# Performance work log

Measured on AMD Instinct MI355X. Metric: run time of the kernel, lower is better.

The kernel has to match this reference:

```python
import jax, jax.numpy as jnp
import numpy as np

A, E, O = 8, 4096, 256          # agents, envs-per-agent, obs dim
H1, H2, H3 = 1024, 1024, 512     # idims
S = 4                            # number of shared (SEPS) networks


def setup_inputs() -> dict:
    key = jax.random.key(0)
    ks = jax.random.split(key, 8)
    f32 = jnp.float32
    return {
        "x": jax.random.normal(ks[0], (A, E, O), f32),
        "W1": jax.random.normal(ks[1], (S, O, H1), f32) * (1.0 / np.sqrt(O)),
        "b1": jnp.zeros((S, H1), f32),
        "W2": jax.random.normal(ks[2], (S, H1, H2), f32) * (np.sqrt(2.0) / np.sqrt(H1)),
        "b2": jnp.zeros((S, H2), f32),
        "W3": jax.random.normal(ks[3], (S, H2, H3), f32) * (np.sqrt(2.0) / np.sqrt(H2)),
        "b3": jnp.zeros((S, H3), f32),
        "seps_idx": jax.random.randint(ks[4], (A,), 0, S, dtype=jnp.int64),
    }


def reference(x, W1, b1, W2, b2, W3, b3, seps_idx):
    # x: [A, E, O]. Each of the S nets is applied (as in the original Python
    # loop) to the full stacked input, then the per-agent output is gathered
    # by seps_idx. MLP: Linear -> ReLU -> Linear -> ReLU -> Linear.
    def mlp(w1, bb1, w2, bb2, w3, bb3):
        h = jax.nn.relu(jnp.einsum('aeo,oh->aeh', x, w1) + bb1)
        h = jax.nn.relu(jnp.einsum('aeh,hg->aeg', h, w2) + bb2)
        return jnp.einsum('aeg,gk->aek', h, w3) + bb3

    out = jax.vmap(mlp)(W1, b1, W2, b2, W3, b3)           # [S, A, E, H3]
    sel = out[seps_idx, jnp.arange(A)]                    # [A, E, H3]
    return sel
```

## Files before the change

kernel.cpp:

```cpp
#include <hip/hip_runtime.h>
#include <hip/hip_bf16.h>


typedef unsigned short u16;
typedef __bf16 bf16x8 __attribute__((ext_vector_type(8)));
typedef float floatx4 __attribute__((ext_vector_type(4)));
typedef unsigned short ushort8 __attribute__((ext_vector_type(8)));

__device__ __forceinline__ u16 f2bf(float f) {
    union { float f; unsigned int u; } v; v.f = f;
    unsigned int u = v.u;
    return (u16)((u + 0x7FFFu + ((u >> 16) & 1u)) >> 16);
}

__device__ __forceinline__ void load16(const void* g, void* l) {
    __builtin_amdgcn_global_load_lds(
        (const __attribute__((address_space(1))) void*)(unsigned long long)g,
        (__attribute__((address_space(3))) void*)(unsigned int)(unsigned long long)l,
        16, 0, 0);
}

__global__ __launch_bounds__(256) void prep(
    const float* __restrict__ x, u16* __restrict__ xb,
    const float* __restrict__ W1, u16* __restrict__ w1t,
    const float* __restrict__ W2, u16* __restrict__ w2t,
    const float* __restrict__ W3, u16* __restrict__ w3t) {
    __shared__ float tile[32][33];
    int b = blockIdx.x;
    const int tid = threadIdx.x;
    if (b < 8192) {
        int i = (b * 256 + tid) * 4;
        float4 v = *(const float4*)(x + i);
        ushort4 o;
        o.x = f2bf(v.x); o.y = f2bf(v.y); o.z = f2bf(v.z); o.w = f2bf(v.w);
        *(ushort4*)(xb + i) = o;
        return;
    }
    b -= 8192;
    const float* src; u16* dst; int K, N, n0, k0, s;
    if (b < 1024) {
        s = b >> 8; int r = b & 255;
        K = 256; N = 1024; n0 = (r & 31) * 32; k0 = (r >> 5) * 32;
        src = W1; dst = w1t;
    } else if (b < 5120) {
        b -= 1024; s = b >> 10; int r = b & 1023;
        K = 1024; N = 1024; n0 = (r & 31) * 32; k0 = (r >> 5) * 32;
        src = W2; dst = w2t;
    } else {
        b -= 5120; s = b >> 9; int r = b & 511;
        K = 1024; N = 512; n0 = (r & 15) * 32; k0 = (r >> 4) * 32;
        src = W3; dst = w3t;
    }
    src += (size_t)s * K * N;
    dst += (size_t)s * N * K;
    const int tx = tid & 31, ty = tid >> 5;
#pragma unroll
    for (int j = 0; j < 32; j += 8)
        tile[ty + j][tx] = src[(size_t)(k0 + ty + j) * N + (n0 + tx)];
    __syncthreads();
#pragma unroll
    for (int j = 0; j < 32; j += 8)
        dst[(size_t)(n0 + ty + j) * K + (k0 + tx)] = f2bf(tile[tx][ty + j]);
}

template <int K, int N, bool RELU, bool OUT_BF16>
__global__ __launch_bounds__(512, 2) void gemm_mlp(
    const u16* __restrict__ Amat, const u16* __restrict__ Wt,
    const float* __restrict__ bias, const int* __restrict__ seps,
    void* __restrict__ outp) {
    constexpr int BM = 256, BK = 32;
    constexpr int NT = K / BK;
    constexpr int NHT = 4 * NT;
    constexpr int NNB = N / 256;
    constexpr int LNB = (NNB == 4) ? 2 : 1;
    extern __shared__ u16 lds[];

    const int tid = threadIdx.x;
    const int wave = tid >> 6, lane = tid & 63;
    const int wm = wave >> 2, wn = wave & 3;
    const int quad = lane >> 4, l16 = lane & 15;

    const int bidx = blockIdx.x;
    const int t = bidx >> 3;
    const int mb = (t >> LNB) * 8 + (bidx & 7);
    const int nb = t & (NNB - 1);
    const int m0 = mb * BM, n0 = nb * 256;

    const int s = seps[m0 >> 12];
    const u16* Ab = Amat + (size_t)m0 * K;
    const u16* Bb = Wt + ((size_t)s * N + n0) * K;

    const int soff = ((wave << 4) + (lane >> 2)) * K
                   + (((lane & 3) ^ ((lane >> 2) & 3)) << 3);
    u16* const ldsw = &lds[wave << 9];

    auto STAGE = [&](int sh) {
        if (sh < NHT) {
            const int tl = sh >> 2, ht = sh & 3;
            const u16* g = (ht & 2) ? Bb : Ab;
            if (ht & 1) g += 128 * K;
            load16(g + tl * BK + soff, ldsw + ((tl & 3) << 14) + (ht << 12));
        }
    };

    floatx4 acc[8][4];
#pragma unroll
    for (int i = 0; i < 8; ++i)
#pragma unroll
        for (int j = 0; j < 4; ++j) acc[i][j] = (floatx4){0.f, 0.f, 0.f, 0.f};

#pragma unroll
    for (int sh = 0; sh < 8; ++sh) STAGE(sh);
    asm volatile("s_waitcnt vmcnt(4)" ::: "memory");
    __builtin_amdgcn_s_barrier();

    const int aslot = (quad ^ (l16 & 3)) << 3;
    const int arow = (wm << 7) + l16;
    const int brow = (wn << 6) + l16;

#pragma unroll 1
    for (int T = 0; T < NT; ++T) {
        const u16* buf = &lds[(T & 3) << 14];
        const int sb = (T + 2) << 2;
        bf16x8 bfr[4];
#pragma unroll
        for (int q = 0; q < 2; ++q) {
            bf16x8 af[4];
#pragma unroll
            for (int i = 0; i < 4; ++i)
                af[i] = *(const bf16x8*)&buf[((arow + (q << 6) + (i << 4)) << 5) + aslot];
            if (q == 0) {
#pragma unroll
                for (int nf = 0; nf < 4; ++nf)
                    bfr[nf] = *(const bf16x8*)&buf[8192 + ((brow + (nf << 4)) << 5) + aslot];
            }
            STAGE(sb + (q << 1));
            STAGE(sb + (q << 1) + 1);
            if (q == 1) {
                if (T < NT - 2) asm volatile("s_waitcnt vmcnt(4)" ::: "memory");
                else            asm volatile("s_waitcnt vmcnt(0)" ::: "memory");
            }
            __builtin_amdgcn_s_barrier();
            asm volatile("s_waitcnt lgkmcnt(0)" ::: "memory");
            __builtin_amdgcn_sched_barrier(0);
            __builtin_amdgcn_s_setprio(1);
#pragma unroll
            for (int i = 0; i < 4; ++i)
#pragma unroll
                for (int nf = 0; nf < 4; ++nf)
                    acc[(q << 2) + i][nf] = __builtin_amdgcn_mfma_f32_16x16x32_bf16(
                        af[i], bfr[nf], acc[(q << 2) + i][nf], 0, 0, 0);
            __builtin_amdgcn_s_setprio(0);
            __builtin_amdgcn_sched_barrier(0);
            __builtin_amdgcn_s_barrier();
        }
    }
    __syncthreads();

    float* eps = (float*)lds;
    constexpr int EW = 268;
    float bv[4];
#pragma unroll
    for (int nf = 0; nf < 4; ++nf)
        bv[nf] = bias[s * N + n0 + (wn << 6) + (nf << 4) + l16];

    const int rL = tid & 63;
    const int rw = tid >> 6;

#pragma unroll
    for (int mf = 0; mf < 8; ++mf) {
#pragma unroll
        for (int nf = 0; nf < 4; ++nf)
#pragma unroll
            for (int r = 0; r < 4; ++r) {
                float v = acc[mf][nf][r] + bv[nf];
                if (RELU) v = fmaxf(v, 0.0f);
                eps[((wm << 4) + (quad << 2) + r) * EW + (wn << 6) + (nf << 4) + l16] = v;
            }
        __syncthreads();
#pragma unroll
        for (int j = 0; j < 4; ++j) {
            const int er = rw + (j << 3);
            const int grow = m0 + ((er >> 4) << 7) + (mf << 4) + (er & 15);
            const float4 v = *(const float4*)&eps[er * EW + (rL << 2)];
            if (OUT_BF16) {
                ushort4 o;
                o.x = f2bf(v.x); o.y = f2bf(v.y); o.z = f2bf(v.z); o.w = f2bf(v.w);
                *(ushort4*)((u16*)outp + (size_t)grow * N + n0 + (rL << 2)) = o;
            } else {
                *(float4*)((float*)outp + (size_t)grow * N + n0 + (rL << 2)) = v;
            }
        }
        __syncthreads();
    }
}

extern "C" void kernel_launch(void* const* d_in, const int* in_sizes, int n_in,
                              void* d_out, int out_size, void* d_ws, size_t ws_size,
                              hipStream_t stream) {
    const float* x  = (const float*)d_in[0];
    const float* W1 = (const float*)d_in[1];
    const float* b1 = (const float*)d_in[2];
    const float* W2 = (const float*)d_in[3];
    const float* b2 = (const float*)d_in[4];
    const float* W3 = (const float*)d_in[5];
    const float* b3 = (const float*)d_in[6];
    const int* seps = (const int*)d_in[7];

    char* ws = (char*)d_ws;
    u16* w1t = (u16*)(ws);
    u16* w2t = (u16*)(ws + (2ull << 20));
    u16* w3t = (u16*)(ws + (10ull << 20));
    u16* xb  = (u16*)(ws + (14ull << 20));
    u16* h1  = (u16*)(ws + (30ull << 20));
    u16* h2  = (u16*)(ws + (94ull << 20));

    static int attr_once = []() {
        auto k1 = gemm_mlp<256, 1024, true, true>;
        auto k2 = gemm_mlp<1024, 1024, true, true>;
        auto k3 = gemm_mlp<1024, 512, false, false>;
        hipFuncSetAttribute(reinterpret_cast<const void*>(k1),
                            hipFuncAttributeMaxDynamicSharedMemorySize, 131072);
        hipFuncSetAttribute(reinterpret_cast<const void*>(k2),
                            hipFuncAttributeMaxDynamicSharedMemorySize, 131072);
        hipFuncSetAttribute(reinterpret_cast<const void*>(k3),
                            hipFuncAttributeMaxDynamicSharedMemorySize, 131072);
        return 0;
    }();
    (void)attr_once;

    prep<<<15360, 256, 0, stream>>>(x, xb, W1, w1t, W2, w2t, W3, w3t);

    gemm_mlp<256, 1024, true, true><<<512, 512, 131072, stream>>>(xb, w1t, b1, seps, h1);
    gemm_mlp<1024, 1024, true, true><<<512, 512, 131072, stream>>>(h1, w2t, b2, seps, h2);
    gemm_mlp<1024, 512, false, false><<<256, 512, 131072, stream>>>(h2, w3t, b3, seps, d_out);
}
```

Before: 278.0 us.

## Switch GEMM mainloop to BK=64 double-buffered tiles with four-phase MFMA schedule

Doubles the K-tile from 32 to 64 and replaces the four-deep, quarter-tile staging pipeline with two 64 KB LDS buffers, each filled in one burst per iteration. The inner loop is split into four phases that reuse A and B fragments across the 2x2 quadrant order, which halves the number of loop iterations and barriers per K. The LDS swizzle is widened to 8 chunks to match the longer rows. In exchange, prefetch depth drops to one tile ahead, so global-load latency is less hidden.

```diff
diff --git a/kernel.cpp b/kernel.cpp
--- a/kernel.cpp
+++ b/kernel.cpp
@@ -5,7 +5,6 @@
 typedef unsigned short u16;
 typedef __bf16 bf16x8 __attribute__((ext_vector_type(8)));
 typedef float floatx4 __attribute__((ext_vector_type(4)));
-typedef unsigned short ushort8 __attribute__((ext_vector_type(8)));
 
 __device__ __forceinline__ u16 f2bf(float f) {
     union { float f; unsigned int u; } v; v.f = f;
@@ -63,14 +62,49 @@
         dst[(size_t)(n0 + ty + j) * K + (k0 + tx)] = f2bf(tile[tx][ty + j]);
 }
 
+#define LDA(H)                                                                 \
+    {                                                                          \
+        _Pragma("unroll") for (int i = 0; i < 4; ++i)                          \
+            _Pragma("unroll") for (int kk = 0; kk < 2; ++kk)                   \
+                af[i][kk] = *(const bf16x8*)&buf[arow0 + ((H) << 12) +         \
+                                                 (i << 10) + cs[kk]];          \
+    }
+
+#define LDB(V, BF)                                                             \
+    {                                                                          \
+        _Pragma("unroll") for (int j = 0; j < 2; ++j)                          \
+            _Pragma("unroll") for (int kk = 0; kk < 2; ++kk)                   \
+                BF[j][kk] = *(const bf16x8*)&buf[16384 + brow0 +               \
+                                                 ((((V) << 1) + j) << 10) +    \
+                                                 cs[kk]];                      \
+    }
+
+#define PHASE(H, V, BF, VM)                                                    \
+    {                                                                          \
+        __builtin_amdgcn_s_barrier();                                          \
+        asm volatile("s_waitcnt lgkmcnt(0)" ::: "memory");                     \
+        __builtin_amdgcn_sched_barrier(0);                                     \
+        __builtin_amdgcn_s_setprio(1);                                         \
+        _Pragma("unroll") for (int i = 0; i < 4; ++i)                          \
+            _Pragma("unroll") for (int j = 0; j < 2; ++j)                      \
+                _Pragma("unroll") for (int kk = 0; kk < 2; ++kk)               \
+                    acc[((H) << 2) + i][((V) << 1) + j] =                      \
+                        __builtin_amdgcn_mfma_f32_16x16x32_bf16(               \
+                            af[i][kk], BF[j][kk],                              \
+                            acc[((H) << 2) + i][((V) << 1) + j], 0, 0, 0);     \
+        __builtin_amdgcn_s_setprio(0);                                         \
+        __builtin_amdgcn_sched_barrier(0);                                     \
+        if (VM) asm volatile("s_waitcnt vmcnt(0)" ::: "memory");               \
+        __builtin_amdgcn_s_barrier();                                          \
+    }
+
 template <int K, int N, bool RELU, bool OUT_BF16>
 __global__ __launch_bounds__(512, 2) void gemm_mlp(
     const u16* __restrict__ Amat, const u16* __restrict__ Wt,
     const float* __restrict__ bias, const int* __restrict__ seps,
     void* __restrict__ outp) {
-    constexpr int BM = 256, BK = 32;
+    constexpr int BK = 64;
     constexpr int NT = K / BK;
-    constexpr int NHT = 4 * NT;
     constexpr int NNB = N / 256;
     constexpr int LNB = (NNB == 4) ? 2 : 1;
     extern __shared__ u16 lds[];
@@ -84,76 +118,61 @@
     const int t = bidx >> 3;
     const int mb = (t >> LNB) * 8 + (bidx & 7);
     const int nb = t & (NNB - 1);
-    const int m0 = mb * BM, n0 = nb * 256;
+    const int m0 = mb * 256, n0 = nb * 256;
 
     const int s = seps[m0 >> 12];
     const u16* Ab = Amat + (size_t)m0 * K;
     const u16* Bb = Wt + ((size_t)s * N + n0) * K;
 
-    const int soff = ((wave << 4) + (lane >> 2)) * K
-                   + (((lane & 3) ^ ((lane >> 2) & 3)) << 3);
-    u16* const ldsw = &lds[wave << 9];
-
-    auto STAGE = [&](int sh) {
-        if (sh < NHT) {
-            const int tl = sh >> 2, ht = sh & 3;
-            const u16* g = (ht & 2) ? Bb : Ab;
-            if (ht & 1) g += 128 * K;
-            load16(g + tl * BK + soff, ldsw + ((tl & 3) << 14) + (ht << 12));
+    const int srow = (wave << 3) + (lane >> 3);
+    const int sch = ((lane & 7) ^ (lane >> 3)) << 3;
+    const u16* gA = Ab + (size_t)srow * K + sch;
+    const u16* gB = Bb + (size_t)srow * K + sch;
+    const unsigned lsw = (unsigned)(wave << 9);
+
+    auto STAGE = [&](int T1) {
+        u16* dbuf = &lds[(T1 & 1) << 15];
+        const int k0 = T1 * BK;
+#pragma unroll
+        for (int cj = 0; cj < 4; ++cj) {
+            load16(gA + (size_t)(cj << 6) * K + k0, dbuf + (cj << 12) + lsw);
+            load16(gB + (size_t)(cj << 6) * K + k0,
+                   dbuf + 16384 + (cj << 12) + lsw);
         }
     };
 
+    const int arow0 = ((wm << 7) + l16) << 6;
+    const int brow0 = ((wn << 6) + l16) << 6;
+    int cs[2];
+    cs[0] = ((quad ^ (l16 & 7)) << 3);
+    cs[1] = (((4 + quad) ^ (l16 & 7)) << 3);
+
     floatx4 acc[8][4];
 #pragma unroll
     for (int i = 0; i < 8; ++i)
 #pragma unroll
         for (int j = 0; j < 4; ++j) acc[i][j] = (floatx4){0.f, 0.f, 0.f, 0.f};
 
-#pragma unroll
-    for (int sh = 0; sh < 8; ++sh) STAGE(sh);
-    asm volatile("s_waitcnt vmcnt(4)" ::: "memory");
+    STAGE(0);
+    asm volatile("s_waitcnt vmcnt(0)" ::: "memory");
     __builtin_amdgcn_s_barrier();
 
-    const int aslot = (quad ^ (l16 & 3)) << 3;
-    const int arow = (wm << 7) + l16;
-    const int brow = (wn << 6) + l16;
+    bf16x8 af[4][2], bf0[2][2], bf1[2][2];
 
 #pragma unroll 1
     for (int T = 0; T < NT; ++T) {
-        const u16* buf = &lds[(T & 3) << 14];
-        const int sb = (T + 2) << 2;
-        bf16x8 bfr[4];
-#pragma unroll
-        for (int q = 0; q < 2; ++q) {
-            bf16x8 af[4];
-#pragma unroll
-            for (int i = 0; i < 4; ++i)
-                af[i] = *(const bf16x8*)&buf[((arow + (q << 6) + (i << 4)) << 5) + aslot];
-            if (q == 0) {
-#pragma unroll
-                for (int nf = 0; nf < 4; ++nf)
-                    bfr[nf] = *(const bf16x8*)&buf[8192 + ((brow + (nf << 4)) << 5) + aslot];
-            }
-            STAGE(sb + (q << 1));
-            STAGE(sb + (q << 1) + 1);
-            if (q == 1) {
-                if (T < NT - 2) asm volatile("s_waitcnt vmcnt(4)" ::: "memory");
-                else            asm volatile("s_waitcnt vmcnt(0)" ::: "memory");
-            }
-            __builtin_amdgcn_s_barrier();
-            asm volatile("s_waitcnt lgkmcnt(0)" ::: "memory");
-            __builtin_amdgcn_sched_barrier(0);
-            __builtin_amdgcn_s_setprio(1);
-#pragma unroll
-            for (int i = 0; i < 4; ++i)
-#pragma unroll
-                for (int nf = 0; nf < 4; ++nf)
-                    acc[(q << 2) + i][nf] = __builtin_amdgcn_mfma_f32_16x16x32_bf16(
-                        af[i], bfr[nf], acc[(q << 2) + i][nf], 0, 0, 0);
-            __builtin_amdgcn_s_setprio(0);
-            __builtin_amdgcn_sched_barrier(0);
-            __builtin_amdgcn_s_barrier();
-        }
+        const u16* buf = &lds[(T & 1) << 15];
+        const bool more = (T + 1 < NT);
+
+        LDA(0);
+        LDB(0, bf0);
+        if (more) STAGE(T + 1);
+        PHASE(0, 0, bf0, false);
+        LDB(1, bf1);
+        PHASE(0, 1, bf1, false);
+        LDA(1);
+        PHASE(1, 1, bf1, false);
+        PHASE(1, 0, bf0, more);
     }
     __syncthreads();
 
```

Result: faster. 265.2 us (-4.6%).

## Restructure GEMM main loop into 3-deep prefetch with one barrier per K-step

Applied to the files above, without the earlier changes.

Replaces the half-tile staging scheme with a 4-buffer ring that prefetches three K-steps ahead. Each step now issues a whole 32-wide A/B tile, waits once with vmcnt and uses a single barrier per iteration instead of several. All 8 A and 4 B fragments are loaded before 32 back-to-back MFMAs. The LDS swizzle changes to XOR on (row>>1)&3 to suit the new store layout. This aims to cut barrier and wait overhead and deepen latency hiding, at the cost of more live fragment registers and tighter vmcnt accounting.

```diff
diff --git a/kernel.cpp b/kernel.cpp
--- a/kernel.cpp
+++ b/kernel.cpp
@@ -5,7 +5,6 @@
 typedef unsigned short u16;
 typedef __bf16 bf16x8 __attribute__((ext_vector_type(8)));
 typedef float floatx4 __attribute__((ext_vector_type(4)));
-typedef unsigned short ushort8 __attribute__((ext_vector_type(8)));
 
 __device__ __forceinline__ u16 f2bf(float f) {
     union { float f; unsigned int u; } v; v.f = f;
@@ -63,14 +62,15 @@
         dst[(size_t)(n0 + ty + j) * K + (k0 + tx)] = f2bf(tile[tx][ty + j]);
 }
 
+#define VMCNT(n) asm volatile("s_waitcnt vmcnt(" #n ")" ::: "memory")
+#define SB0 __builtin_amdgcn_sched_barrier(0)
+
 template <int K, int N, bool RELU, bool OUT_BF16>
 __global__ __launch_bounds__(512, 2) void gemm_mlp(
     const u16* __restrict__ Amat, const u16* __restrict__ Wt,
     const float* __restrict__ bias, const int* __restrict__ seps,
     void* __restrict__ outp) {
-    constexpr int BM = 256, BK = 32;
-    constexpr int NT = K / BK;
-    constexpr int NHT = 4 * NT;
+    constexpr int P = K / 32;
     constexpr int NNB = N / 256;
     constexpr int LNB = (NNB == 4) ? 2 : 1;
     extern __shared__ u16 lds[];
@@ -84,76 +84,69 @@
     const int t = bidx >> 3;
     const int mb = (t >> LNB) * 8 + (bidx & 7);
     const int nb = t & (NNB - 1);
-    const int m0 = mb * BM, n0 = nb * 256;
+    const int m0 = mb * 256, n0 = nb * 256;
 
     const int s = seps[m0 >> 12];
     const u16* Ab = Amat + (size_t)m0 * K;
     const u16* Bb = Wt + ((size_t)s * N + n0) * K;
 
-    const int soff = ((wave << 4) + (lane >> 2)) * K
-                   + (((lane & 3) ^ ((lane >> 2) & 3)) << 3);
-    u16* const ldsw = &lds[wave << 9];
-
-    auto STAGE = [&](int sh) {
-        if (sh < NHT) {
-            const int tl = sh >> 2, ht = sh & 3;
-            const u16* g = (ht & 2) ? Bb : Ab;
-            if (ht & 1) g += 128 * K;
-            load16(g + tl * BK + soff, ldsw + ((tl & 3) << 14) + (ht << 12));
+    const int srow = (wave << 5) + (lane >> 2);
+    const int gsw = (((lane & 3) ^ ((lane >> 3) & 3)) << 3);
+    const u16* gA = Ab + (size_t)srow * K + gsw;
+    const u16* gB = Bb + (size_t)srow * K + gsw;
+    const unsigned lw = (unsigned)(wave << 10);
+
+    auto STAGE = [&](int p) {
+        u16* ub = &lds[(p & 3) << 14];
+        const int kо = p << 5;
+#pragma unroll
+        for (int j = 0; j < 2; ++j) {
+            load16(gA + (size_t)(j << 4) * K + kо, ub + lw + (j << 9));
+            load16(gB + (size_t)(j << 4) * K + kо, ub + 8192 + lw + (j << 9));
         }
     };
 
+    const int sA = (quad ^ ((l16 >> 1) & 3)) << 3;
+    const int a0 = (((wm << 7) + l16) << 5) + sA;
+    const int b0 = 8192 + (((wn << 6) + l16) << 5) + sA;
+
     floatx4 acc[8][4];
 #pragma unroll
     for (int i = 0; i < 8; ++i)
 #pragma unroll
         for (int j = 0; j < 4; ++j) acc[i][j] = (floatx4){0.f, 0.f, 0.f, 0.f};
 
-#pragma unroll
-    for (int sh = 0; sh < 8; ++sh) STAGE(sh);
-    asm volatile("s_waitcnt vmcnt(4)" ::: "memory");
-    __builtin_amdgcn_s_barrier();
-
-    const int aslot = (quad ^ (l16 & 3)) << 3;
-    const int arow = (wm << 7) + l16;
-    const int brow = (wn << 6) + l16;
+    STAGE(0); STAGE(1); STAGE(2);
+
+    bf16x8 af[8], bf[4];
 
 #pragma unroll 1
-    for (int T = 0; T < NT; ++T) {
-        const u16* buf = &lds[(T & 3) << 14];
-        const int sb = (T + 2) << 2;
-        bf16x8 bfr[4];
-#pragma unroll
-        for (int q = 0; q < 2; ++q) {
-            bf16x8 af[4];
-#pragma unroll
-            for (int i = 0; i < 4; ++i)
-                af[i] = *(const bf16x8*)&buf[((arow + (q << 6) + (i << 4)) << 5) + aslot];
-            if (q == 0) {
-#pragma unroll
-                for (int nf = 0; nf < 4; ++nf)
-                    bfr[nf] = *(const bf16x8*)&buf[8192 + ((brow + (nf << 4)) << 5) + aslot];
-            }
-            STAGE(sb + (q << 1));
-            STAGE(sb + (q << 1) + 1);
-            if (q == 1) {
-                if (T < NT - 2) asm volatile("s_waitcnt vmcnt(4)" ::: "memory");
-                else            asm volatile("s_waitcnt vmcnt(0)" ::: "memory");
-            }
-            __builtin_amdgcn_s_barrier();
-            asm volatile("s_waitcnt lgkmcnt(0)" ::: "memory");
-            __builtin_amdgcn_sched_barrier(0);
-            __builtin_amdgcn_s_setprio(1);
-#pragma unroll
-            for (int i = 0; i < 4; ++i)
-#pragma unroll
-                for (int nf = 0; nf < 4; ++nf)
-                    acc[(q << 2) + i][nf] = __builtin_amdgcn_mfma_f32_16x16x32_bf16(
-                        af[i], bfr[nf], acc[(q << 2) + i][nf], 0, 0, 0);
-            __builtin_amdgcn_s_setprio(0);
-            __builtin_amdgcn_sched_barrier(0);
-            __builtin_amdgcn_s_barrier();
-        }
+    for (int p = 0; p < P; ++p) {
+        if (p <= P - 3)      { VMCNT(8); }
+        else if (p == P - 2) { VMCNT(4); }
+        else                 { VMCNT(0); }
+        SB0;
+        __builtin_amdgcn_s_barrier();
+        SB0;
+
+        const u16* buf = &lds[(p & 3) << 14];
+        if (p + 3 < P) STAGE(p + 3);
+        af[0] = *(const bf16x8*)&buf[a0];
+#pragma unroll
+        for (int nf = 0; nf < 4; ++nf)
+            bf[nf] = *(const bf16x8*)&buf[b0 + (nf << 9)];
+#pragma unroll
+        for (int i = 1; i < 8; ++i)
+            af[i] = *(const bf16x8*)&buf[a0 + (i << 9)];
+
+        __builtin_amdgcn_s_setprio(1);
+#pragma unroll
+        for (int i = 0; i < 8; ++i)
+#pragma unroll
+            for (int nf = 0; nf < 4; ++nf)
+                acc[i][nf] = __builtin_amdgcn_mfma_f32_16x16x32_bf16(
+                    af[i], bf[nf], acc[i][nf], 0, 0, 0);
+        __builtin_amdgcn_s_setprio(0);
     }
     __syncthreads();
 
```

New measurement: 264.5 us. 1.05x faster.
